# Kernel tuning notes

Hardware: AMD Instinct MI355X
Metric: run time of the kernel (lower is better)

## Reference

```python
import jax, jax.numpy as jnp
import numpy as np

NUM_GRAPHS = 256
BN_EPS = 1e-5


def _bn(x, g, b, m, v):
    # eval-mode BatchNorm1d: affine with running stats
    return (x - m) * jax.lax.rsqrt(v + BN_EPS) * g + b


def setup_inputs() -> dict:
    key = jax.random.key(0)
    ks = jax.random.split(key, 16)
    N = 500_000
    x = jax.random.normal(ks[0], (N, 3), dtype=jnp.float32)
    batch = jnp.sort(jax.random.randint(ks[1], (N,), 0, NUM_GRAPHS, dtype=jnp.int32))

    def lin(k, fan_in, fan_out):
        kw, kb = jax.random.split(k)
        s = 1.0 / np.sqrt(fan_in)
        W = jax.random.uniform(kw, (fan_in, fan_out), jnp.float32, -s, s)
        b = jax.random.uniform(kb, (fan_out,), jnp.float32, -s, s)
        return W, b

    def bn_params(k, dim):
        k1, k2, k3, k4 = jax.random.split(k, 4)
        g = 1.0 + 0.05 * jax.random.normal(k1, (dim,), jnp.float32)
        be = 0.05 * jax.random.normal(k2, (dim,), jnp.float32)
        m = 0.05 * jax.random.normal(k3, (dim,), jnp.float32)
        v = 0.5 + jax.random.uniform(k4, (dim,), jnp.float32)
        return g, be, m, v

    W1, b1 = lin(ks[2], 3, 64)
    g1, be1, m1, v1 = bn_params(ks[3], 64)
    W2, b2 = lin(ks[4], 64, 64)          # plain last layer of local MLP
    W3, b3 = lin(ks[5], 64, 128)
    g3, be3, m3, v3 = bn_params(ks[6], 128)
    W4, b4 = lin(ks[7], 128, 1024)       # plain last layer of global MLP

    return {
        "x": x, "batch": batch,
        "W1": W1, "b1": b1, "g1": g1, "be1": be1, "m1": m1, "v1": v1,
        "W2": W2, "b2": b2,
        "W3": W3, "b3": b3, "g3": g3, "be3": be3, "m3": m3, "v3": v3,
        "W4": W4, "b4": b4,
    }


def reference(x, batch, W1, b1, g1, be1, m1, v1, W2, b2,
              W3, b3, g3, be3, m3, v3, W4, b4):
    # local MLP [3, 64, 64]: Linear->BN->ReLU, plain last
    h = jax.nn.relu(_bn(x @ W1 + b1, g1, be1, m1, v1))   # [N, 64]
    h = h @ W2 + b2                                       # [N, 64]
    # global MLP [64, 128, 1024]: Linear->BN->ReLU, plain last
    h = jax.nn.relu(_bn(h @ W3 + b3, g3, be3, m3, v3))    # [N, 128]
    h = h @ W4 + b4                                       # [N, 1024]
    # global_max_pool: ragged scatter-max over per-point graph ids
    out = jax.ops.segment_max(h, batch, num_segments=NUM_GRAPHS)  # [G, 1024]
    return out
```

## Files before the change

### kernel.cpp

```cpp
#include <hip/hip_runtime.h>
#include <hip/hip_bf16.h>
#include <cstdint>

typedef __attribute__((ext_vector_type(8))) short bf16x8;
typedef __attribute__((ext_vector_type(4))) float f32x4;

#define BN_EPS 1e-5f

__device__ __forceinline__ unsigned short f2bf(float f) {
    unsigned int u = __float_as_uint(f);
    unsigned int r = (u + 0x7FFFu + ((u >> 16) & 1u)) >> 16;
    return (unsigned short)r;
}
__device__ __forceinline__ float bf2f(unsigned short h) {
    return __uint_as_float(((unsigned int)h) << 16);
}
__device__ __forceinline__ unsigned int encf(float f) {
    unsigned int u = __float_as_uint(f);
    return (u & 0x80000000u) ? ~u : (u | 0x80000000u);
}
__device__ __forceinline__ float decf(unsigned int e) {
    return __uint_as_float((e & 0x80000000u) ? (e & 0x7FFFFFFFu) : ~e);
}

__device__ __forceinline__ long long lbound(const int* __restrict__ b, long long n, int key) {
    long long lo = 0, hi = n;
    while (lo < hi) { long long mid = (lo + hi) >> 1; if (b[mid] < key) lo = mid + 1; else hi = mid; }
    return lo;
}

__global__ void fold_kernel(const float* __restrict__ W1, const float* __restrict__ b1,
                            const float* __restrict__ g1, const float* __restrict__ be1,
                            const float* __restrict__ m1, const float* __restrict__ v1,
                            const float* __restrict__ W2, const float* __restrict__ b2,
                            const float* __restrict__ W3, const float* __restrict__ b3,
                            const float* __restrict__ g3, const float* __restrict__ be3,
                            const float* __restrict__ m3, const float* __restrict__ v3,
                            const float* __restrict__ W4,
                            unsigned short* __restrict__ W4p,
                            unsigned short* __restrict__ W23ph, unsigned short* __restrict__ W23pl,
                            float* __restrict__ W1c, float* __restrict__ b23,
                            unsigned int* __restrict__ out, int out_size) {
    int tid = blockIdx.x * blockDim.x + threadIdx.x;
    if (tid < 131072) {
        int j = tid & 7, lane = (tid >> 3) & 63, kf = (tid >> 9) & 3, nt = tid >> 11;
        int col = nt * 16 + (lane & 15);
        int k = kf * 32 + (lane >> 4) * 8 + j;
        W4p[tid] = f2bf(W4[k * 1024 + col]);
    }
    if (tid < out_size) out[tid] = 0x007FFFFFu;
    if (tid + 131072 < out_size) out[tid + 131072] = 0x007FFFFFu;
    if (tid < 8192) {
        int j = tid & 7, lane = (tid >> 3) & 63, kf = (tid >> 9) & 1, nn = tid >> 10;
        int col = nn * 16 + (lane & 15);
        int k = kf * 32 + (lane >> 4) * 8 + j;
        float s3 = g3[col] / sqrtf(v3[col] + BN_EPS);
        float acc = 0.f;
        for (int o = 0; o < 64; ++o) acc += W2[k * 64 + o] * W3[o * 128 + col];
        float w = acc * s3;
        unsigned short hi = f2bf(w);
        W23ph[tid] = hi;
        W23pl[tid] = f2bf(w - bf2f(hi));
    }
    if (tid < 128) {
        float s3 = g3[tid] / sqrtf(v3[tid] + BN_EPS);
        float acc = b3[tid] - m3[tid];
        for (int o = 0; o < 64; ++o) acc += b2[o] * W3[o * 128 + tid];
        b23[tid] = acc * s3 + be3[tid];
    }
    if (tid < 256) {
        int o = tid >> 2, c = tid & 3;
        float s1 = g1[o] / sqrtf(v1[o] + BN_EPS);
        W1c[tid] = (c < 3) ? W1[c * 64 + o] * s1 : (b1[o] - m1[o]) * s1 + be1[o];
    }
}

__global__ __launch_bounds__(128, 4) void fused_kernel(const float* __restrict__ x,
                                                       const float* __restrict__ W1c,
                                                       const unsigned short* __restrict__ W23ph,
                                                       const unsigned short* __restrict__ W23pl,
                                                       const float* __restrict__ b23,
                                                       const unsigned short* __restrict__ W4p,
                                                       const float* __restrict__ b4,
                                                       const int* __restrict__ batch,
                                                       unsigned int* __restrict__ out,
                                                       float* __restrict__ tilemax,
                                                       int* __restrict__ gtile,
                                                       long long pbase, int ntiles, long long Ntot) {
    __shared__ unsigned short h3s[2][64 * 72];
    int wave = blockIdx.x * 2 + (threadIdx.x >> 6);
    if (wave >= ntiles) return;
    unsigned short* h3 = h3s[threadIdx.x >> 6];
    int lane = threadIdx.x & 63;
    int q = lane >> 4, r16 = lane & 15;
    long long p0 = pbase + (long long)wave * 64;

    float xv[4][3];
    bool valid[4];
#pragma unroll
    for (int mt = 0; mt < 4; ++mt) {
        long long p = p0 + mt * 16 + r16;
        if (p < Ntot) {
            xv[mt][0] = x[p * 3 + 0]; xv[mt][1] = x[p * 3 + 1]; xv[mt][2] = x[p * 3 + 2];
            valid[mt] = true;
        } else {
            xv[mt][0] = xv[mt][1] = xv[mt][2] = 0.f; valid[mt] = false;
        }
    }
    bf16x8 a2[4][2];
#pragma unroll
    for (int kf = 0; kf < 2; ++kf)
#pragma unroll
        for (int j = 0; j < 8; ++j) {
            int f = kf * 32 + q * 8 + j;
            float4 w = *reinterpret_cast<const float4*>(W1c + f * 4);
#pragma unroll
            for (int mt = 0; mt < 4; ++mt) {
                float v = fmaf(xv[mt][0], w.x, fmaf(xv[mt][1], w.y, fmaf(xv[mt][2], w.z, w.w)));
                v = valid[mt] ? fmaxf(v, 0.f) : 0.f;
                a2[mt][kf][j] = (short)f2bf(v);
            }
        }

    bf16x8 a[4][4];
#pragma unroll
    for (int half = 0; half < 2; ++half) {
#pragma unroll
        for (int n = 0; n < 4; ++n) {
            int nn = half * 4 + n;
            f32x4 acc2[4];
#pragma unroll
            for (int mt = 0; mt < 4; ++mt) acc2[mt] = (f32x4){0.f, 0.f, 0.f, 0.f};
#pragma unroll
            for (int kf = 0; kf < 2; ++kf) {
                bf16x8 bh = *reinterpret_cast<const bf16x8*>(W23ph + (size_t)((nn * 2 + kf) * 64 + lane) * 8);
                bf16x8 bl = *reinterpret_cast<const bf16x8*>(W23pl + (size_t)((nn * 2 + kf) * 64 + lane) * 8);
#pragma unroll
                for (int mt = 0; mt < 4; ++mt) {
                    acc2[mt] = __builtin_amdgcn_mfma_f32_16x16x32_bf16(a2[mt][kf], bh, acc2[mt], 0, 0, 0);
                    acc2[mt] = __builtin_amdgcn_mfma_f32_16x16x32_bf16(a2[mt][kf], bl, acc2[mt], 0, 0, 0);
                }
            }
            int col = nn * 16 + r16;
            float bias = b23[col];
#pragma unroll
            for (int mt = 0; mt < 4; ++mt)
#pragma unroll
                for (int r = 0; r < 4; ++r) {
                    int row = mt * 16 + q * 4 + r;
                    float v = fmaxf(acc2[mt][r] + bias, 0.f);
                    h3[row * 72 + n * 16 + r16] = f2bf(v);
                }
        }
        asm volatile("s_waitcnt lgkmcnt(0)" ::: "memory");
#pragma unroll
        for (int mt = 0; mt < 4; ++mt)
#pragma unroll
            for (int kfl = 0; kfl < 2; ++kfl)
                a[mt][half * 2 + kfl] =
                    *reinterpret_cast<const bf16x8*>(h3 + (16 * mt + r16) * 72 + kfl * 32 + q * 8);
        asm volatile("s_waitcnt lgkmcnt(0)" ::: "memory");
    }

    long long plast = p0 + 63; if (plast > Ntot - 1) plast = Ntot - 1;
    int gfirst = batch[(p0 < Ntot) ? p0 : (Ntot - 1)];
    int glast = batch[plast];
    bool fast = (gfirst == glast) && (p0 + 63 < Ntot);
    if (lane == 0) gtile[wave] = fast ? gfirst : -1;

    if (fast) {
        float* tm = tilemax + (size_t)wave * 1024;
        const unsigned short* wp = W4p + (size_t)lane * 8;
        bf16x8 Bp[2][4];
#pragma unroll
        for (int kf = 0; kf < 4; ++kf)
            Bp[0][kf] = *reinterpret_cast<const bf16x8*>(wp + (size_t)kf * 512);

        for (int g8 = 0; g8 < 8; ++g8) {
            float m8[8];
#pragma unroll
            for (int i8 = 0; i8 < 8; ++i8) {
                int nt = g8 * 8 + i8;
                const int cur = i8 & 1, nxt = cur ^ 1;
                {
                    const unsigned short* wq = wp + (size_t)(((nt + 1) & 63) * 4) * 512;
#pragma unroll
                    for (int kf = 0; kf < 4; ++kf)
                        Bp[nxt][kf] = *reinterpret_cast<const bf16x8*>(wq + (size_t)kf * 512);
                }
                f32x4 acc[4];
#pragma unroll
                for (int mt = 0; mt < 4; ++mt) acc[mt] = (f32x4){0.f, 0.f, 0.f, 0.f};
#pragma unroll
                for (int kf = 0; kf < 4; ++kf)
#pragma unroll
                    for (int mt = 0; mt < 4; ++mt)
                        acc[mt] = __builtin_amdgcn_mfma_f32_16x16x32_bf16(a[mt][kf], Bp[cur][kf], acc[mt], 0, 0, 0);
                float m = fmaxf(fmaxf(fmaxf(acc[0][0], acc[0][1]), fmaxf(acc[0][2], acc[0][3])),
                                fmaxf(fmaxf(acc[1][0], acc[1][1]), fmaxf(acc[1][2], acc[1][3])));
                m = fmaxf(m, fmaxf(fmaxf(fmaxf(acc[2][0], acc[2][1]), fmaxf(acc[2][2], acc[2][3])),
                                   fmaxf(fmaxf(acc[3][0], acc[3][1]), fmaxf(acc[3][2], acc[3][3]))));
                m8[i8] = m;
            }
#pragma unroll
            for (int qq = 0; qq < 8; ++qq) {
                float v = m8[qq];
                v = fmaxf(v, __shfl_xor(v, 16));
                v = fmaxf(v, __shfl_xor(v, 32));
                m8[qq] = v;
            }
            if (lane < 16) {
#pragma unroll
                for (int qq = 0; qq < 8; ++qq) tm[(g8 * 8 + qq) * 16 + lane] = m8[qq];
            }
        }
        return;
    }

    int gl = -1;
    unsigned long long smask = 0;
    int grow[16];
    {
        long long pl = p0 + lane;
        gl = (pl < Ntot) ? batch[pl] : -1;
        int gprev = __shfl_up(gl, 1);
        bool is_start = (lane == 0) || (gl != gprev);
        smask = __ballot(is_start);
#pragma unroll
        for (int m = 0; m < 4; ++m)
#pragma unroll
            for (int r = 0; r < 4; ++r) {
                int rw = m * 16 + (lane >> 4) * 4 + r;
                grow[m * 4 + r] = __shfl(gl, rw);
            }
    }

    for (int nt = 0; nt < 64; ++nt) {
        bf16x8 bq[4];
#pragma unroll
        for (int kf = 0; kf < 4; ++kf)
            bq[kf] = *reinterpret_cast<const bf16x8*>(W4p + (size_t)((nt * 4 + kf) * 64 + lane) * 8);
        f32x4 acc[4];
#pragma unroll
        for (int m = 0; m < 4; ++m) acc[m] = (f32x4){0.f, 0.f, 0.f, 0.f};
#pragma unroll
        for (int kf = 0; kf < 4; ++kf)
#pragma unroll
            for (int m = 0; m < 4; ++m)
                acc[m] = __builtin_amdgcn_mfma_f32_16x16x32_bf16(a[m][kf], bq[kf], acc[m], 0, 0, 0);

        int col = nt * 16 + (lane & 15);
        float bias = b4[col];
        unsigned long long tmp = smask;
        while (tmp) {
            int ls = __builtin_ctzll(tmp); tmp &= tmp - 1;
            int gs = __shfl(gl, ls);
            float m = -INFINITY;
#pragma unroll
            for (int mm = 0; mm < 4; ++mm)
#pragma unroll
                for (int r = 0; r < 4; ++r)
                    if (grow[mm * 4 + r] == gs) m = fmaxf(m, acc[mm][r]);
            m = fmaxf(m, __shfl_xor(m, 16));
            m = fmaxf(m, __shfl_xor(m, 32));
            if (gs >= 0 && lane < 16 && m > -INFINITY)
                atomicMax(&out[gs * 1024 + col], encf(m + bias));
        }
    }
}

__global__ __launch_bounds__(256) void reduce_chunk(const float* __restrict__ tilemax,
                                                    const int* __restrict__ gtile,
                                                    const int* __restrict__ batch,
                                                    const float* __restrict__ b4,
                                                    unsigned int* __restrict__ out,
                                                    long long base, long long npts, long long N,
                                                    int finalize) {
    int g = blockIdx.x >> 2;
    int col = (blockIdx.x & 3) * 256 + threadIdx.x;
    __shared__ int sh[2];
    if (threadIdx.x == 0) {
        long long lo = lbound(batch, N, g);
        long long hi = lbound(batch, N, g + 1);
        long long e = base + npts;
        if (lo < base) lo = base;
        if (hi > e) hi = e;
        sh[0] = (int)(lo - base);
        sh[1] = (int)(hi - base);
    }
    __syncthreads();
    int lo = sh[0], hi = sh[1];
    if (!finalize && lo >= hi) return;
    float m = -INFINITY;
    if (lo < hi) {
        int t0 = lo >> 6, t1 = (hi - 1) >> 6;
        for (int t = t0; t <= t1; ++t)
            if (gtile[t] == g) m = fmaxf(m, tilemax[(size_t)t * 1024 + col]);
    }
    int idx = g * 1024 + col;
    if (finalize) {
        float cur = decf(out[idx]);
        if (m > -INFINITY) cur = fmaxf(cur, m + b4[col]);
        out[idx] = __float_as_uint(cur);
    } else {
        if (m > -INFINITY) atomicMax(&out[idx], encf(m + b4[col]));
    }
}

extern "C" void kernel_launch(void* const* d_in, const int* in_sizes, int n_in,
                              void* d_out, int out_size, void* d_ws, size_t ws_size,
                              hipStream_t stream) {
    const float* x   = (const float*)d_in[0];
    const int* batch = (const int*)d_in[1];
    const float* W1  = (const float*)d_in[2];
    const float* b1  = (const float*)d_in[3];
    const float* g1  = (const float*)d_in[4];
    const float* be1 = (const float*)d_in[5];
    const float* m1  = (const float*)d_in[6];
    const float* v1  = (const float*)d_in[7];
    const float* W2  = (const float*)d_in[8];
    const float* b2  = (const float*)d_in[9];
    const float* W3  = (const float*)d_in[10];
    const float* b3  = (const float*)d_in[11];
    const float* g3  = (const float*)d_in[12];
    const float* be3 = (const float*)d_in[13];
    const float* m3  = (const float*)d_in[14];
    const float* v3  = (const float*)d_in[15];
    const float* W4  = (const float*)d_in[16];
    const float* b4  = (const float*)d_in[17];

    long long N = in_sizes[1];

    char* ws = (char*)d_ws;
    unsigned short* W4p   = (unsigned short*)(ws + 0);
    unsigned short* W23ph = (unsigned short*)(ws + 262144);
    unsigned short* W23pl = (unsigned short*)(ws + 278528);
    float* W1c = (float*)(ws + 294912);
    float* b23 = (float*)(ws + 295936);

    fold_kernel<<<512, 256, 0, stream>>>(W1, b1, g1, be1, m1, v1, W2, b2, W3, b3, g3, be3, m3, v3,
                                         W4, W4p, W23ph, W23pl, W1c, b23,
                                         (unsigned int*)d_out, out_size);

    const size_t ofs = 1 << 20;
    size_t avail = (ws_size > ofs) ? ws_size - ofs : 0;
    long long Tcap = (long long)(avail / 4104);
    Tcap &= ~3LL;
    if (Tcap < 4) Tcap = 4;
    long long ntiles_tot = (N + 63) / 64;
    long long ntcap = (ntiles_tot + 3) & ~3LL;
    if (Tcap > ntcap) Tcap = ntcap;

    float* tilemax = (float*)(ws + ofs);
    int* gtile = (int*)(ws + ofs + (size_t)Tcap * 4096);
    long long chunk = Tcap * 64;

    for (long long base = 0; base < N; base += chunk) {
        long long npts = N - base; if (npts > chunk) npts = chunk;
        int ntiles = (int)((npts + 63) / 64);
        int blocks = (ntiles + 1) / 2;
        fused_kernel<<<blocks, 128, 0, stream>>>(x, W1c, W23ph, W23pl, b23, W4p, b4, batch,
                                                 (unsigned int*)d_out, tilemax, gtile,
                                                 base, ntiles, N);
        int finalize = (base + chunk >= N) ? 1 : 0;
        reduce_chunk<<<1024, 256, 0, stream>>>(tilemax, gtile, batch, b4, (unsigned int*)d_out,
                                               base, npts, N, finalize);
    }
}
```

Baseline: 205.0 us.

## Stream W4 fragments through LDS with a triple-buffered async global_load_lds pipeline

In the single-graph fast path, W4 B-fragments were previously double-buffered in registers. They are now fetched with global_load_lds into a three-stage ring in shared memory, with vmcnt waits keeping two tiles in flight. Each stage is read back from LDS before its MFMAs. The intent is to hide global load latency further ahead and cut VGPR pressure. In exchange it adds LDS round trips, waitcnt stalls, and a larger shared allocation per block, which could limit occupancy.

```diff
diff --git a/kernel.cpp b/kernel.cpp
--- a/kernel.cpp
+++ b/kernel.cpp
@@ -27,6 +27,12 @@
     long long lo = 0, hi = n;
     while (lo < hi) { long long mid = (lo + hi) >> 1; if (b[mid] < key) lo = mid + 1; else hi = mid; }
     return lo;
+}
+
+__device__ __forceinline__ void gl_lds16(const unsigned short* g, unsigned short* l) {
+    __builtin_amdgcn_global_load_lds((const __attribute__((address_space(1))) unsigned int*)g,
+                                     (__attribute__((address_space(3))) unsigned int*)l,
+                                     16, 0, 0);
 }
 
 __global__ void fold_kernel(const float* __restrict__ W1, const float* __restrict__ b1,
@@ -87,10 +93,10 @@
                                                        float* __restrict__ tilemax,
                                                        int* __restrict__ gtile,
                                                        long long pbase, int ntiles, long long Ntot) {
-    __shared__ unsigned short h3s[2][64 * 72];
+    __shared__ unsigned short ldss[2][6144];
     int wave = blockIdx.x * 2 + (threadIdx.x >> 6);
     if (wave >= ntiles) return;
-    unsigned short* h3 = h3s[threadIdx.x >> 6];
+    unsigned short* h3 = ldss[threadIdx.x >> 6];
     int lane = threadIdx.x & 63;
     int q = lane >> 4, r16 = lane & 15;
     long long p0 = pbase + (long long)wave * 64;
@@ -170,24 +176,25 @@
 
     if (fast) {
         float* tm = tilemax + (size_t)wave * 1024;
-        const unsigned short* wp = W4p + (size_t)lane * 8;
-        bf16x8 Bp[2][4];
-#pragma unroll
-        for (int kf = 0; kf < 4; ++kf)
-            Bp[0][kf] = *reinterpret_cast<const bf16x8*>(wp + (size_t)kf * 512);
-
+#pragma unroll
+        for (int t = 0; t < 3; ++t)
+#pragma unroll
+            for (int kf = 0; kf < 4; ++kf)
+                gl_lds16(W4p + (size_t)((t * 4 + kf) * 512) + lane * 8,
+                         h3 + t * 2048 + kf * 512);
+
+        int s = 0;
         for (int g8 = 0; g8 < 8; ++g8) {
             float m8[8];
 #pragma unroll
             for (int i8 = 0; i8 < 8; ++i8) {
                 int nt = g8 * 8 + i8;
-                const int cur = i8 & 1, nxt = cur ^ 1;
-                {
-                    const unsigned short* wq = wp + (size_t)(((nt + 1) & 63) * 4) * 512;
-#pragma unroll
-                    for (int kf = 0; kf < 4; ++kf)
-                        Bp[nxt][kf] = *reinterpret_cast<const bf16x8*>(wq + (size_t)kf * 512);
-                }
+                asm volatile("s_waitcnt vmcnt(8)" ::: "memory");
+                const unsigned short* bb = h3 + s * 2048 + lane * 8;
+                bf16x8 bq[4];
+#pragma unroll
+                for (int kf = 0; kf < 4; ++kf)
+                    bq[kf] = *reinterpret_cast<const bf16x8*>(bb + kf * 512);
                 f32x4 acc[4];
 #pragma unroll
                 for (int mt = 0; mt < 4; ++mt) acc[mt] = (f32x4){0.f, 0.f, 0.f, 0.f};
@@ -195,12 +202,21 @@
                 for (int kf = 0; kf < 4; ++kf)
 #pragma unroll
                     for (int mt = 0; mt < 4; ++mt)
-                        acc[mt] = __builtin_amdgcn_mfma_f32_16x16x32_bf16(a[mt][kf], Bp[cur][kf], acc[mt], 0, 0, 0);
+                        acc[mt] = __builtin_amdgcn_mfma_f32_16x16x32_bf16(a[mt][kf], bq[kf], acc[mt], 0, 0, 0);
                 float m = fmaxf(fmaxf(fmaxf(acc[0][0], acc[0][1]), fmaxf(acc[0][2], acc[0][3])),
                                 fmaxf(fmaxf(acc[1][0], acc[1][1]), fmaxf(acc[1][2], acc[1][3])));
                 m = fmaxf(m, fmaxf(fmaxf(fmaxf(acc[2][0], acc[2][1]), fmaxf(acc[2][2], acc[2][3])),
                                    fmaxf(fmaxf(acc[3][0], acc[3][1]), fmaxf(acc[3][2], acc[3][3]))));
                 m8[i8] = m;
+                asm volatile("s_waitcnt lgkmcnt(0)" ::: "memory");
+                {
+                    int ntn = (nt + 3) & 63;
+#pragma unroll
+                    for (int kf = 0; kf < 4; ++kf)
+                        gl_lds16(W4p + (size_t)((ntn * 4 + kf) * 512) + lane * 8,
+                                 h3 + s * 2048 + kf * 512);
+                }
+                s = (s == 2) ? 0 : s + 1;
             }
 #pragma unroll
             for (int qq = 0; qq < 8; ++qq) {
```

Result: slower. 233.3 us (+13.8%).
